# Kernel optimization log

Hardware: AMD Instinct MI355X
Metric: run time of the kernel (lower is better)

## Reference

```python
import jax, jax.numpy as jnp
import numpy as np
from jax import lax


def conv2d(x, w, b, stride=1, pad=0):
    y = lax.conv_general_dilated(x, w, (stride, stride), [(pad, pad), (pad, pad)],
                                 dimension_numbers=('NCHW', 'OIHW', 'NCHW'))
    return y + b[None, :, None, None]


def squash(s, axis):
    # v = (|s|^2 / (1+|s|^2)) * s / |s|
    sq = jnp.sum(s * s, axis=axis, keepdims=True)
    return (sq / (1.0 + sq)) * s / jnp.sqrt(sq + 1e-9)


def conv_capsule(x, w, b_conv, caps_bias, out_dim, out_atoms, num_routing, stride, pad):
    # x: [B, in_dim, in_atoms, H, W]
    B, in_dim, in_atoms, H, W = x.shape
    xr = x.reshape(B * in_dim, in_atoms, H, W)
    conv = conv2d(xr, w, b_conv, stride, pad)              # [B*in_dim, out_dim*out_atoms, Ho, Wo]
    Ho, Wo = conv.shape[-2], conv.shape[-1]
    votes = conv.reshape(B, in_dim, out_dim, out_atoms, Ho, Wo)
    logits = jnp.zeros((B, in_dim, out_dim, Ho, Wo), dtype=x.dtype)
    act = None
    for i in range(num_routing):  # num_routing is a small static int (1 or 3)
        route = jax.nn.softmax(logits, axis=2)             # coupling over output capsules
        preact = jnp.einsum('bioHW,bioaHW->boaHW', route, votes) + caps_bias[None]
        act = squash(preact, axis=2)                        # [B, out_dim, out_atoms, Ho, Wo]
        if i < num_routing - 1:
            logits = logits + jnp.einsum('bioaHW,boaHW->bioHW', votes, act)
    return act


def forward(x, y, W1, b1, Wp, bp, cbp, Ws, bs, cbs, Wr1, br1, Wr2, br2, Wr3, br3):
    conv1 = jax.nn.relu(conv2d(x, W1, b1, 1, 2))                       # [B,256,H,W]
    primary = conv_capsule(conv1[:, None], Wp, bp, cbp, 32, 8, 1, 1, 2)  # [B,32,8,H,W]
    seg = conv_capsule(primary, Ws, bs, cbs, 1, 16, 3, 1, 0)             # [B,1,16,H,W]
    out_seg = jnp.sqrt(jnp.sum(seg * seg, axis=2) + 1e-9)                # Length: [B,1,H,W]
    masked = seg * y[:, :, None]                                         # Mask by label
    B, C, A, H, W = masked.shape
    r = masked.reshape(B * C, A, H, W)                                   # [B,16,H,W]
    r = jax.nn.relu(conv2d(r, Wr1, br1))
    r = jax.nn.relu(conv2d(r, Wr2, br2))
    out_recon = jax.nn.sigmoid(conv2d(r, Wr3, br3))                      # [B,1,H,W]
    return out_seg, out_recon


def setup_inputs():
    key = jax.random.key(0)
    ks = jax.random.split(key, 10)
    B, H, W = 2, 128, 128
    s = 0.05
    return {
        'x': jax.random.uniform(ks[0], (B, 1, H, W), jnp.float32),
        'y': (jax.random.uniform(ks[1], (B, 1, H, W)) > 0.5).astype(jnp.float32),
        'W1': jax.random.normal(ks[2], (256, 1, 5, 5), jnp.float32) * s,
        'b1': jnp.zeros((256,), jnp.float32),
        'Wp': jax.random.normal(ks[3], (256, 256, 5, 5), jnp.float32) * 0.01,
        'bp': jnp.zeros((256,), jnp.float32),
        'cbp': jnp.full((32, 8, 1, 1), 0.1, jnp.float32),
        'Ws': jax.random.normal(ks[4], (16, 8, 1, 1), jnp.float32) * s,
        'bs': jnp.zeros((16,), jnp.float32),
        'cbs': jnp.full((1, 16, 1, 1), 0.1, jnp.float32),
        'Wr1': jax.random.normal(ks[5], (64, 16, 1, 1), jnp.float32) * s,
        'br1': jnp.zeros((64,), jnp.float32),
        'Wr2': jax.random.normal(ks[6], (128, 64, 1, 1), jnp.float32) * s,
        'br2': jnp.zeros((128,), jnp.float32),
        'Wr3': jax.random.normal(ks[7], (1, 128, 1, 1), jnp.float32) * s,
        'br3': jnp.zeros((1,), jnp.float32),
    }


def reference(x, y, W1, b1, Wp, bp, cbp, Ws, bs, cbs, Wr1, br1, Wr2, br2, Wr3, br3):
    return forward(x, y, W1, b1, Wp, bp, cbp, Ws, bs, cbs, Wr1, br1, Wr2, br2, Wr3, br3)
```

## Files before the change

kernel.cpp:

```cpp
#include <hip/hip_runtime.h>
#include <hip/hip_bf16.h>

typedef __attribute__((ext_vector_type(8))) unsigned short us8;
typedef __attribute__((ext_vector_type(8))) __bf16 bf16x8;
typedef __attribute__((ext_vector_type(4))) float f32x4;

__device__ __forceinline__ unsigned short f2bf(float f) {
  unsigned int u = __float_as_uint(f);
  u += 0x7FFFu + ((u >> 16) & 1u);
  return (unsigned short)(u >> 16);
}
__device__ __forceinline__ float bf2f(unsigned short u) {
  return __uint_as_float(((unsigned int)u) << 16);
}

__device__ __forceinline__ void gld16(const unsigned short* g, unsigned short* l) {
  __builtin_amdgcn_global_load_lds(reinterpret_cast<const unsigned int*>(g),
                                   reinterpret_cast<unsigned int*>(l), 16, 0, 0);
}

#define APAD_BYTES 17842176
#define BT_OFF     17842176
#define PP_OFF     21118976

__global__ __launch_bounds__(256) void prep_halo(const float* __restrict__ Wp,
                                                 unsigned short* __restrict__ BT,
                                                 unsigned short* __restrict__ Apad) {
  __shared__ float w[6400];
  const int bid = blockIdx.x, tid = threadIdx.x;
  if (bid < 256) {
    const float* src = Wp + bid * 6400;
    for (int i = tid; i < 6400; i += 256) w[i] = src[i];
    __syncthreads();
    for (int k = tid; k < 6400; k += 256) {
      int dhw = k >> 8, c = k & 255;
      BT[bid * 6400 + k] = f2bf(w[c * 25 + dhw]);
    }
  } else {
    int idx = (bid - 256) * 256 + tid;
    int chunk = idx & 31;
    int pix = idx >> 5;
    int img = pix >= 1040;
    int p = pix - img * 1040;
    int h, w2;
    if (p < 528) {
      int rs = p / 132;
      h = (rs < 2) ? rs : rs + 128;
      w2 = p - rs * 132;
    } else {
      int q = p - 528;
      h = 2 + (q >> 2);
      int cs = q & 3;
      w2 = (cs < 2) ? cs : cs + 128;
    }
    us8 z = {0, 0, 0, 0, 0, 0, 0, 0};
    *(us8*)(Apad + (size_t)(img * 17424 + h * 132 + w2) * 256 + chunk * 8) = z;
  }
}

__global__ __launch_bounds__(256) void conv1_k(const float* __restrict__ x,
                                               const float* __restrict__ W1,
                                               const float* __restrict__ b1,
                                               unsigned short* __restrict__ Apad) {
  int t = threadIdx.x;
  int pxt = blockIdx.x >> 3;
  int cq  = blockIdx.x & 7;
  int px  = (pxt << 6) + (t & 63);
  int cg  = __builtin_amdgcn_readfirstlane(t >> 6);
  int co0 = (cq << 5) + (cg << 3);
  int b = px >> 14, hw = px & 16383;
  int h = hw >> 7, w = hw & 127;

  float patch[25];
#pragma unroll
  for (int dh = 0; dh < 5; ++dh)
#pragma unroll
    for (int dw = 0; dw < 5; ++dw) {
      int hh = h + dh - 2, ww = w + dw - 2;
      bool ok = (hh >= 0) & (hh < 128) & (ww >= 0) & (ww < 128);
      patch[dh * 5 + dw] = ok ? x[(b << 14) + hh * 128 + ww] : 0.f;
    }
  us8 o;
#pragma unroll
  for (int c = 0; c < 8; ++c) {
    float acc = b1[co0 + c];
#pragma unroll
    for (int i = 0; i < 25; ++i) acc += patch[i] * W1[(co0 + c) * 25 + i];
    o[c] = f2bf(fmaxf(acc, 0.f));
  }
  *(us8*)(Apad + (size_t)((b * 132 + h + 2) * 132 + (w + 2)) * 256 + co0) = o;
}

#define STAGE_A(slot, ku) do { int dhw_=(ku)>>3, dh_=dhw_/5, dw_=dhw_-dh_*5;   \
    int ao_=((dh_*132+dw_)<<8)+(((ku)&7)<<5);                                  \
    gld16(Aap+abase0+ao_, &As[slot][sA]);                                      \
    gld16(Aap+abase1+ao_, &As[slot][sA+4096]); } while(0)
#define STAGE_B(slot, ku) do { int kp_=(ku)<<5;                                \
    gld16(BT+bbase0+kp_, &Bs[slot][sA]);                                       \
    gld16(BT+bbase1+kp_, &Bs[slot][sA+4096]); } while(0)
#define RDA(slot, s) (*(const bf16x8*)(&As[slot][areadbase + (s)*512]))
#define RDB(slot, j) (*(const bf16x8*)(&Bs[slot][breadbase + (j)*512]))
#define MFMA_Q(aset, bset, rb) do {                                            \
  _Pragma("unroll") for (int s_ = 0; s_ < 4; ++s_)                             \
  _Pragma("unroll") for (int j_ = 0; j_ < 4; ++j_)                             \
    acc[(rb)+s_][j_] = __builtin_amdgcn_mfma_f32_16x16x32_bf16(                \
        aset[s_], bset[j_], acc[(rb)+s_][j_], 0, 0, 0); } while(0)
#define BAR() __builtin_amdgcn_s_barrier()
#define VMC(n) asm volatile("s_waitcnt vmcnt(" #n ")" ::: "memory")

__global__ __launch_bounds__(512, 2) void caps_conv2(
    const unsigned short* __restrict__ Aap,
    const unsigned short* __restrict__ BT,
    unsigned short* __restrict__ Pp)
{
  __shared__ __attribute__((aligned(16))) unsigned short As[4][8192];
  __shared__ __attribute__((aligned(16))) unsigned short Bs[4][8192];

  const int tid = threadIdx.x;
  const int bid = blockIdx.x;
  const int lid = (bid & 7) * 32 + (bid >> 3);
  const int kid = lid & 1;
  const int m0 = (lid >> 1) << 8;
  const int t0 = kid * 100;
  const int wid = tid >> 6;
  const int l = tid & 63;

  const int swz = (l & 3) ^ ((l >> 3) & 3);
  int abase0, abase1, bbase0, bbase1;
  {
    int ra = wid * 16 + (l >> 2);
    int m = m0 + ra;
    int b = m >> 14, hw = m & 16383, h = hw >> 7, w = hw & 127;
    abase0 = ((b * 132 + h) * 132 + w) * 256 + swz * 8;
    m = m0 + ra + 128;
    b = m >> 14; hw = m & 16383; h = hw >> 7; w = hw & 127;
    abase1 = ((b * 132 + h) * 132 + w) * 256 + swz * 8;
    bbase0 = ra * 6400 + swz * 8;
    bbase1 = (ra + 128) * 6400 + swz * 8;
  }
  const int sA = wid * 512;

  const int rl = l & 15, q = l >> 4;
  const int wm = wid >> 2, wn = wid & 3;
  const int areadbase = (wm * 128 + rl) * 32 + ((q ^ ((rl >> 1) & 3)) << 3);
  const int breadbase = (wn * 64 + rl) * 32 + ((q ^ ((rl >> 1) & 3)) << 3);

  f32x4 acc[8][4] = {};
  bf16x8 aL[2][4], aH[4], bB[2][4];

  STAGE_A(0, t0 + 0); STAGE_B(0, t0 + 0);
  STAGE_A(1, t0 + 1); STAGE_B(1, t0 + 1);
  STAGE_A(2, t0 + 2); STAGE_B(2, t0 + 2);
  VMC(8); BAR();
#pragma unroll
  for (int s = 0; s < 4; ++s) aL[0][s] = RDA(0, s);
#pragma unroll
  for (int j = 0; j < 4; ++j) bB[0][j] = RDB(0, j);

  for (int it = 0; it < 24; ++it) {
    const int ub = t0 + it * 4;
#pragma unroll
    for (int sub = 0; sub < 4; ++sub) {
      const int par = sub & 1, nxt = par ^ 1;
      const int sU = sub, sU1 = (sub + 1) & 3, sS = (sub + 3) & 3;
#pragma unroll
      for (int s = 0; s < 4; ++s) aH[s] = RDA(sU, 4 + s);
      STAGE_A(sS, ub + sub + 3);
      VMC(6);
#pragma unroll
      for (int j = 0; j < 4; ++j) bB[nxt][j] = RDB(sU1, j);
      BAR();
      __builtin_amdgcn_s_setprio(1);
      MFMA_Q(aL[par], bB[par], 0);
      __builtin_amdgcn_s_setprio(0);
      BAR();
#pragma unroll
      for (int s = 0; s < 4; ++s) aL[nxt][s] = RDA(sU1, s);
      STAGE_B(sS, ub + sub + 3);
      BAR();
      __builtin_amdgcn_s_setprio(1);
      MFMA_Q(aH, bB[par], 4);
      __builtin_amdgcn_s_setprio(0);
      BAR();
    }
  }

#pragma unroll
  for (int s = 0; s < 4; ++s) aH[s] = RDA(0, 4 + s);
  STAGE_A(3, t0 + 99);
  VMC(6);
#pragma unroll
  for (int j = 0; j < 4; ++j) bB[1][j] = RDB(1, j);
  BAR();
  __builtin_amdgcn_s_setprio(1); MFMA_Q(aL[0], bB[0], 0);
  __builtin_amdgcn_s_setprio(0); BAR();
#pragma unroll
  for (int s = 0; s < 4; ++s) aL[1][s] = RDA(1, s);
  STAGE_B(3, t0 + 99);
  BAR();
  __builtin_amdgcn_s_setprio(1); MFMA_Q(aH, bB[0], 4);
  __builtin_amdgcn_s_setprio(0); BAR();
#pragma unroll
  for (int s = 0; s < 4; ++s) aH[s] = RDA(1, 4 + s);
  VMC(4);
#pragma unroll
  for (int j = 0; j < 4; ++j) bB[0][j] = RDB(2, j);
  BAR();
  MFMA_Q(aL[1], bB[1], 0); BAR();
#pragma unroll
  for (int s = 0; s < 4; ++s) aL[0][s] = RDA(2, s);
  BAR();
  MFMA_Q(aH, bB[1], 4); BAR();
#pragma unroll
  for (int s = 0; s < 4; ++s) aH[s] = RDA(2, 4 + s);
  VMC(0);
#pragma unroll
  for (int j = 0; j < 4; ++j) bB[1][j] = RDB(3, j);
  BAR();
  MFMA_Q(aL[0], bB[0], 0); BAR();
#pragma unroll
  for (int s = 0; s < 4; ++s) aL[1][s] = RDA(3, s);
  BAR();
  MFMA_Q(aH, bB[0], 4); BAR();
#pragma unroll
  for (int s = 0; s < 4; ++s) aH[s] = RDA(3, 4 + s);
  MFMA_Q(aL[1], bB[1], 0);
  MFMA_Q(aH, bB[1], 4);

  unsigned short* P = Pp + kid * 8388608;
#pragma unroll
  for (int s = 0; s < 8; ++s) {
#pragma unroll
    for (int j = 0; j < 4; ++j) {
      int col = wn * 64 + j * 16 + rl;
      int mrow = m0 + wm * 128 + s * 16 + (q << 2);
#pragma unroll
      for (int e = 0; e < 4; ++e)
        P[(size_t)(mrow + e) * 256 + col] = f2bf(acc[s][j][e]);
    }
  }
}

__global__ __launch_bounds__(256) void tail_k3(
    const unsigned short* __restrict__ Pp, const float* __restrict__ y,
    const float* __restrict__ bp, const float* __restrict__ cbp,
    const float* __restrict__ Ws, const float* __restrict__ bs,
    const float* __restrict__ cbs,
    const float* __restrict__ Wr1, const float* __restrict__ br1,
    const float* __restrict__ Wr2, const float* __restrict__ br2,
    const float* __restrict__ Wr3, const float* __restrict__ br3,
    float* __restrict__ out) {
  __shared__ float ccl[256];
  __shared__ float sbl[16];
  __shared__ float Wsl[128];
  __shared__ float W1l[1024];
  __shared__ float b1l[64];
  __shared__ float W2l[8192];
  __shared__ float b2l[128];
  __shared__ float W3l[128];

  const int tid = threadIdx.x;
  ccl[tid] = bp[tid] * (1.f / 32.f) + cbp[tid];
  if (tid < 16) sbl[tid] = 32.f * bs[tid] + cbs[tid];
  if (tid < 128) { Wsl[tid] = Ws[tid]; b2l[tid] = br2[tid]; W3l[tid] = Wr3[tid]; }
  if (tid < 64) b1l[tid] = br1[tid];
  for (int i = tid; i < 1024; i += 256) W1l[i] = Wr1[i];
  for (int i = tid; i < 8192; i += 256) W2l[i] = Wr2[i];
  __syncthreads();

  const int m = blockIdx.x * 128 + (tid >> 1);
  const int hf = tid & 1;

  const us8* pr0 = (const us8*)(Pp + (size_t)m * 256) + hf * 16;
  const us8* pr1 = (const us8*)(Pp + 8388608 + (size_t)m * 256) + hf * 16;
  float P8[8] = {0.f, 0.f, 0.f, 0.f, 0.f, 0.f, 0.f, 0.f};
#pragma unroll 4
  for (int i = 0; i < 16; ++i) {
    us8 a = pr0[i], b = pr1[i];
    const int ci = (hf * 16 + i) * 8;
    float v[8];
#pragma unroll
    for (int c = 0; c < 8; ++c)
      v[c] = (bf2f(a[c]) + bf2f(b[c])) * (1.f / 32.f) + ccl[ci + c];
    float sqa = v[0]*v[0] + v[1]*v[1] + v[2]*v[2] + v[3]*v[3];
    float sqb = v[4]*v[4] + v[5]*v[5] + v[6]*v[6] + v[7]*v[7];
    float sq = sqa + sqb;
    float scale = sq / ((1.f + sq) * sqrtf(sq + 1e-9f));
#pragma unroll
    for (int c = 0; c < 8; ++c) P8[c] += v[c] * scale;
  }
#pragma unroll
  for (int c = 0; c < 8; ++c) P8[c] += __shfl_xor(P8[c], 1);

  float pre[16];
  float sqx = 0.f, sqy = 0.f;
#pragma unroll
  for (int a = 0; a < 16; ++a) {
    float s0 = P8[0]*Wsl[a*8+0] + P8[1]*Wsl[a*8+1] + P8[2]*Wsl[a*8+2] + P8[3]*Wsl[a*8+3];
    float s1 = P8[4]*Wsl[a*8+4] + P8[5]*Wsl[a*8+5] + P8[6]*Wsl[a*8+6] + P8[7]*Wsl[a*8+7];
    float s = sbl[a] + s0 + s1;
    pre[a] = s;
    if (a & 1) sqy += s * s; else sqx += s * s;
  }
  float sq2 = sqx + sqy;
  float sc2 = sq2 / ((1.f + sq2) * sqrtf(sq2 + 1e-9f));
  if (hf == 0) out[m] = sqrtf(sq2 * sc2 * sc2 + 1e-9f);

  const float f = sc2 * y[m];
  float r1o[32];
#pragma unroll
  for (int jj = 0; jj < 32; ++jj) {
    const float* wr = W1l + (hf * 32 + jj) * 16;
    float s0 = 0.f, s1 = 0.f;
#pragma unroll
    for (int a = 0; a < 8; ++a) { s0 += pre[a] * f * wr[a]; s1 += pre[a+8] * f * wr[a+8]; }
    r1o[jj] = fmaxf(b1l[hf * 32 + jj] + s0 + s1, 0.f);
  }
  float lo[32], hi[32];
#pragma unroll
  for (int jj = 0; jj < 32; ++jj) {
    float tmp = __shfl_xor(r1o[jj], 1);
    lo[jj] = hf ? tmp : r1o[jj];
    hi[jj] = hf ? r1o[jj] : tmp;
  }
  float a0 = 0.f, a1 = 0.f, a2 = 0.f, a3 = 0.f;
#pragma unroll 4
  for (int kk = 0; kk < 64; ++kk) {
    const int k = hf * 64 + kk;
    const float* w = W2l + k * 64;
    float s0 = 0.f, s1 = 0.f, s2 = 0.f, s3 = 0.f;
#pragma unroll
    for (int j = 0; j < 8; ++j) {
      s0 += lo[j] * w[j];        s1 += lo[j + 8] * w[j + 8];
      s2 += lo[j + 16] * w[j + 16]; s3 += lo[j + 24] * w[j + 24];
    }
#pragma unroll
    for (int j = 0; j < 8; ++j) {
      s0 += hi[j] * w[32 + j];        s1 += hi[j + 8] * w[40 + j];
      s2 += hi[j + 16] * w[48 + j];   s3 += hi[j + 24] * w[56 + j];
    }
    float s = b2l[k] + (s0 + s1) + (s2 + s3);
    float t = fmaxf(s, 0.f) * W3l[k];
    switch (kk & 3) { case 0: a0 += t; break; case 1: a1 += t; break;
                      case 2: a2 += t; break; default: a3 += t; }
  }
  float own = (a0 + a1) + (a2 + a3);
  float acc2 = br3[0] + own + __shfl_xor(own, 1);
  if (hf == 0) out[32768 + m] = 1.f / (1.f + expf(-acc2));
}

extern "C" void kernel_launch(void* const* d_in, const int* in_sizes, int n_in,
                              void* d_out, int out_size, void* d_ws, size_t ws_size,
                              hipStream_t stream) {
  const float* x   = (const float*)d_in[0];
  const float* y   = (const float*)d_in[1];
  const float* W1  = (const float*)d_in[2];
  const float* b1  = (const float*)d_in[3];
  const float* Wp  = (const float*)d_in[4];
  const float* bp  = (const float*)d_in[5];
  const float* cbp = (const float*)d_in[6];
  const float* Ws  = (const float*)d_in[7];
  const float* bs  = (const float*)d_in[8];
  const float* cbs = (const float*)d_in[9];
  const float* Wr1 = (const float*)d_in[10];
  const float* br1 = (const float*)d_in[11];
  const float* Wr2 = (const float*)d_in[12];
  const float* br2 = (const float*)d_in[13];
  const float* Wr3 = (const float*)d_in[14];
  const float* br3 = (const float*)d_in[15];
  float* out = (float*)d_out;

  char* ws = (char*)d_ws;
  unsigned short* Apad = (unsigned short*)ws;
  unsigned short* BT   = (unsigned short*)(ws + BT_OFF);
  unsigned short* Pp   = (unsigned short*)(ws + PP_OFF);

  hipLaunchKernelGGL(prep_halo, dim3(516), dim3(256), 0, stream, Wp, BT, Apad);
  hipLaunchKernelGGL(conv1_k, dim3(4096), dim3(256), 0, stream, x, W1, b1, Apad);
  hipLaunchKernelGGL(caps_conv2, dim3(256), dim3(512), 0, stream, Apad, BT, Pp);
  hipLaunchKernelGGL(tail_k3, dim3(256), dim3(256), 0, stream,
                     Pp, y, bp, cbp, Ws, bs, cbs, Wr1, br1, Wr2, br2, Wr3, br3, out);
}
```

Before: 162.7 us.

## Load B weights directly from global into registers, dropping LDS staging

The weight (B) operand of the implicit-GEMM conv is now read straight from global memory into registers, double-buffered, instead of being staged through LDS. The B shared buffer is removed, halving LDS use per block. The main loop is restructured into two sub-steps per iteration with new barrier and wait placement. This cuts LDS traffic and barriers, but each wave now issues uncoalesced, strided 16-byte global loads of B, and these loads are duplicated across waves that share the same wn.

```diff
diff --git a/kernel.cpp b/kernel.cpp
--- a/kernel.cpp
+++ b/kernel.cpp
@@ -95,18 +95,26 @@
     int ao_=((dh_*132+dw_)<<8)+(((ku)&7)<<5);                                  \
     gld16(Aap+abase0+ao_, &As[slot][sA]);                                      \
     gld16(Aap+abase1+ao_, &As[slot][sA+4096]); } while(0)
-#define STAGE_B(slot, ku) do { int kp_=(ku)<<5;                                \
-    gld16(BT+bbase0+kp_, &Bs[slot][sA]);                                       \
-    gld16(BT+bbase1+kp_, &Bs[slot][sA+4096]); } while(0)
-#define RDA(slot, s) (*(const bf16x8*)(&As[slot][areadbase + (s)*512]))
-#define RDB(slot, j) (*(const bf16x8*)(&Bs[slot][breadbase + (j)*512]))
-#define MFMA_Q(aset, bset, rb) do {                                            \
-  _Pragma("unroll") for (int s_ = 0; s_ < 4; ++s_)                             \
+#define BLOAD(p, u) do { const int kp_ = (t0+(u))<<5;                          \
+    bf[p][0] = *(const bf16x8*)(BT + bbF + kp_);                               \
+    bf[p][1] = *(const bf16x8*)(BT + bbF + 102400 + kp_);                      \
+    bf[p][2] = *(const bf16x8*)(BT + bbF + 204800 + kp_);                      \
+    bf[p][3] = *(const bf16x8*)(BT + bbF + 307200 + kp_); } while(0)
+#define READ_LO(slot) do { _Pragma("unroll") for (int s_ = 0; s_ < 4; ++s_)    \
+    aF[s_] = *(const bf16x8*)(&As[slot][areadbase + s_*512]); } while(0)
+#define READ_HI(slot) do { _Pragma("unroll") for (int s_ = 0; s_ < 4; ++s_)    \
+    aF[4+s_] = *(const bf16x8*)(&As[slot][areadbase + (4+s_)*512]); } while(0)
+#define MF_LO(p) do { _Pragma("unroll") for (int s_ = 0; s_ < 4; ++s_)         \
   _Pragma("unroll") for (int j_ = 0; j_ < 4; ++j_)                             \
-    acc[(rb)+s_][j_] = __builtin_amdgcn_mfma_f32_16x16x32_bf16(                \
-        aset[s_], bset[j_], acc[(rb)+s_][j_], 0, 0, 0); } while(0)
+    acc[s_][j_] = __builtin_amdgcn_mfma_f32_16x16x32_bf16(                     \
+        aF[s_], bf[p][j_], acc[s_][j_], 0, 0, 0); } while(0)
+#define MF_HI(p) do { _Pragma("unroll") for (int s_ = 0; s_ < 4; ++s_)         \
+  _Pragma("unroll") for (int j_ = 0; j_ < 4; ++j_)                             \
+    acc[4+s_][j_] = __builtin_amdgcn_mfma_f32_16x16x32_bf16(                   \
+        aF[4+s_], bf[p][j_], acc[4+s_][j_], 0, 0, 0); } while(0)
 #define BAR() __builtin_amdgcn_s_barrier()
 #define VMC(n) asm volatile("s_waitcnt vmcnt(" #n ")" ::: "memory")
+#define SP(n) __builtin_amdgcn_s_setprio(n)
 
 __global__ __launch_bounds__(512, 2) void caps_conv2(
     const unsigned short* __restrict__ Aap,
@@ -114,7 +122,6 @@
     unsigned short* __restrict__ Pp)
 {
   __shared__ __attribute__((aligned(16))) unsigned short As[4][8192];
-  __shared__ __attribute__((aligned(16))) unsigned short Bs[4][8192];
 
   const int tid = threadIdx.x;
   const int bid = blockIdx.x;
@@ -126,7 +133,7 @@
   const int l = tid & 63;
 
   const int swz = (l & 3) ^ ((l >> 3) & 3);
-  int abase0, abase1, bbase0, bbase1;
+  int abase0, abase1;
   {
     int ra = wid * 16 + (l >> 2);
     int m = m0 + ra;
@@ -135,97 +142,66 @@
     m = m0 + ra + 128;
     b = m >> 14; hw = m & 16383; h = hw >> 7; w = hw & 127;
     abase1 = ((b * 132 + h) * 132 + w) * 256 + swz * 8;
-    bbase0 = ra * 6400 + swz * 8;
-    bbase1 = (ra + 128) * 6400 + swz * 8;
   }
   const int sA = wid * 512;
 
   const int rl = l & 15, q = l >> 4;
   const int wm = wid >> 2, wn = wid & 3;
   const int areadbase = (wm * 128 + rl) * 32 + ((q ^ ((rl >> 1) & 3)) << 3);
-  const int breadbase = (wn * 64 + rl) * 32 + ((q ^ ((rl >> 1) & 3)) << 3);
+  const int bbF = (wn * 64 + rl) * 6400 + q * 8;
 
   f32x4 acc[8][4] = {};
-  bf16x8 aL[2][4], aH[4], bB[2][4];
-
-  STAGE_A(0, t0 + 0); STAGE_B(0, t0 + 0);
-  STAGE_A(1, t0 + 1); STAGE_B(1, t0 + 1);
-  STAGE_A(2, t0 + 2); STAGE_B(2, t0 + 2);
+  bf16x8 aF[8], bf[2][4];
+
+  STAGE_A(0, t0 + 0); STAGE_A(1, t0 + 1); STAGE_A(2, t0 + 2);
+  BLOAD(0, 0);
   VMC(8); BAR();
-#pragma unroll
-  for (int s = 0; s < 4; ++s) aL[0][s] = RDA(0, s);
-#pragma unroll
-  for (int j = 0; j < 4; ++j) bB[0][j] = RDB(0, j);
-
-  for (int it = 0; it < 24; ++it) {
-    const int ub = t0 + it * 4;
-#pragma unroll
-    for (int sub = 0; sub < 4; ++sub) {
-      const int par = sub & 1, nxt = par ^ 1;
-      const int sU = sub, sU1 = (sub + 1) & 3, sS = (sub + 3) & 3;
-#pragma unroll
-      for (int s = 0; s < 4; ++s) aH[s] = RDA(sU, 4 + s);
-      STAGE_A(sS, ub + sub + 3);
-      VMC(6);
-#pragma unroll
-      for (int j = 0; j < 4; ++j) bB[nxt][j] = RDB(sU1, j);
-      BAR();
-      __builtin_amdgcn_s_setprio(1);
-      MFMA_Q(aL[par], bB[par], 0);
-      __builtin_amdgcn_s_setprio(0);
-      BAR();
-#pragma unroll
-      for (int s = 0; s < 4; ++s) aL[nxt][s] = RDA(sU1, s);
-      STAGE_B(sS, ub + sub + 3);
-      BAR();
-      __builtin_amdgcn_s_setprio(1);
-      MFMA_Q(aH, bB[par], 4);
-      __builtin_amdgcn_s_setprio(0);
-      BAR();
-    }
-  }
-
-#pragma unroll
-  for (int s = 0; s < 4; ++s) aH[s] = RDA(0, 4 + s);
+  READ_LO(0); READ_HI(0);
+
+  for (int it = 0; it < 48; ++it) {
+    const int u = it * 2;
+    BLOAD(1, u + 1);
+    STAGE_A((u + 3) & 3, t0 + u + 3);
+    VMC(8); BAR();
+    SP(1); MF_LO(0); SP(0);
+    READ_LO((u + 1) & 3);
+    SP(1); MF_HI(0); SP(0);
+    READ_HI((u + 1) & 3);
+    BAR();
+    BLOAD(0, u + 2);
+    STAGE_A((u + 4) & 3, t0 + u + 4);
+    VMC(8); BAR();
+    SP(1); MF_LO(1); SP(0);
+    READ_LO((u + 2) & 3);
+    SP(1); MF_HI(1); SP(0);
+    READ_HI((u + 2) & 3);
+    BAR();
+  }
+
+  BLOAD(1, 97);
   STAGE_A(3, t0 + 99);
-  VMC(6);
-#pragma unroll
-  for (int j = 0; j < 4; ++j) bB[1][j] = RDB(1, j);
+  VMC(8); BAR();
+  SP(1); MF_LO(0); SP(0);
+  READ_LO(1);
+  SP(1); MF_HI(0); SP(0);
+  READ_HI(1);
   BAR();
-  __builtin_amdgcn_s_setprio(1); MFMA_Q(aL[0], bB[0], 0);
-  __builtin_amdgcn_s_setprio(0); BAR();
-#pragma unroll
-  for (int s = 0; s < 4; ++s) aL[1][s] = RDA(1, s);
-  STAGE_B(3, t0 + 99);
+  BLOAD(0, 98);
+  VMC(6); BAR();
+  SP(1); MF_LO(1); SP(0);
+  READ_LO(2);
+  SP(1); MF_HI(1); SP(0);
+  READ_HI(2);
   BAR();
-  __builtin_amdgcn_s_setprio(1); MFMA_Q(aH, bB[0], 4);
-  __builtin_amdgcn_s_setprio(0); BAR();
-#pragma unroll
-  for (int s = 0; s < 4; ++s) aH[s] = RDA(1, 4 + s);
-  VMC(4);
-#pragma unroll
-  for (int j = 0; j < 4; ++j) bB[0][j] = RDB(2, j);
+  BLOAD(1, 99);
+  VMC(8); BAR();
+  SP(1); MF_LO(0); SP(0);
+  READ_LO(3);
+  SP(1); MF_HI(0); SP(0);
+  READ_HI(3);
   BAR();
-  MFMA_Q(aL[1], bB[1], 0); BAR();
-#pragma unroll
-  for (int s = 0; s < 4; ++s) aL[0][s] = RDA(2, s);
-  BAR();
-  MFMA_Q(aH, bB[1], 4); BAR();
-#pragma unroll
-  for (int s = 0; s < 4; ++s) aH[s] = RDA(2, 4 + s);
-  VMC(0);
-#pragma unroll
-  for (int j = 0; j < 4; ++j) bB[1][j] = RDB(3, j);
-  BAR();
-  MFMA_Q(aL[0], bB[0], 0); BAR();
-#pragma unroll
-  for (int s = 0; s < 4; ++s) aL[1][s] = RDA(3, s);
-  BAR();
-  MFMA_Q(aH, bB[0], 4); BAR();
-#pragma unroll
-  for (int s = 0; s < 4; ++s) aH[s] = RDA(3, 4 + s);
-  MFMA_Q(aL[1], bB[1], 0);
-  MFMA_Q(aH, bB[1], 4);
+  MF_LO(1);
+  MF_HI(1);
 
   unsigned short* P = Pp + kid * 8388608;
 #pragma unroll
```

Result: slower. 215.9 us (+32.7%).
